# Kernel optimization log

Hardware: AMD Instinct MI355X
Metric: run time of the kernel (lower is better)

Reference implementation:

```python
import jax, jax.numpy as jnp
import numpy as np
from jax import lax

D_MODEL = 2048
D_INNER = 4096  # expand * d_model
D_CONV = 4
B, T = 4, 2048


def _rmsnorm(h):
    # F.normalize(x, dim=-1) * sqrt(D): x / max(||x||_2, 1e-12) * sqrt(D)
    n = jnp.sqrt(jnp.sum(h * h, axis=-1, keepdims=True))
    return h / jnp.maximum(n, 1e-12) * (h.shape[-1] ** 0.5)


def setup_inputs() -> dict:
    key = jax.random.key(0)
    ks = jax.random.split(key, 7)
    std = 0.02
    return {
        "x": jax.random.normal(ks[0], (B, T, D_MODEL), jnp.float32),
        "W_in": jax.random.normal(ks[1], (2 * D_INNER, D_MODEL), jnp.float32) * std,
        "conv_w": jax.random.normal(ks[2], (D_INNER, 1, D_CONV), jnp.float32) * std,
        "conv_b": jnp.zeros((D_INNER,), jnp.float32),
        "W_out": jax.random.normal(ks[3], (D_MODEL, D_INNER), jnp.float32) * std,
        "W_mlp1": jax.random.normal(ks[4], (4 * D_MODEL, D_MODEL), jnp.float32) * std,
        "W_mlp2": jax.random.normal(ks[5], (D_MODEL, 4 * D_MODEL), jnp.float32) * std,
    }


def _mamba_fallback(h, W_in, conv_w, conv_b, W_out):
    # in_proj: (B,T,D) -> (B,T,2*d_inner), split into x branch and gate z
    xz = jnp.einsum("btd,ed->bte", h, W_in)
    xp, z = jnp.split(xz, 2, axis=-1)
    # depthwise causal conv over time: torch pads (d_conv-1) both sides then slices [:T]
    # == left-pad-only causal cross-correlation
    xc = lax.conv_general_dilated(
        xp.transpose(0, 2, 1),  # (B, d_inner, T)
        conv_w,                  # (d_inner, 1, d_conv)
        window_strides=(1,),
        padding=[(D_CONV - 1, 0)],
        dimension_numbers=("NCH", "OIH", "NCH"),
        feature_group_count=D_INNER,
    ) + conv_b[None, :, None]
    xc = xc.transpose(0, 2, 1)  # (B, T, d_inner)
    y = jax.nn.silu(xc) * jax.nn.silu(z)
    return jnp.einsum("bte,de->btd", y, W_out)


def reference(x, W_in, conv_w, conv_b, W_out, W_mlp1, W_mlp2):
    # full-dimension path (active_dim=None)
    h = _rmsnorm(x)
    x = x + _mamba_fallback(h, W_in, conv_w, conv_b, W_out)
    h = _rmsnorm(x)
    m = jnp.einsum("bte,de->btd", jax.nn.relu(jnp.einsum("btd,ed->bte", h, W_mlp1)), W_mlp2)
    return x + m
```

## Files before the change

kernel.cpp:

```cpp
#include <hip/hip_runtime.h>
#include <hip/hip_bf16.h>

typedef __bf16 bf16;
typedef __bf16 bf16x8 __attribute__((ext_vector_type(8)));
typedef __bf16 bf16x4 __attribute__((ext_vector_type(4)));
typedef float f32x4 __attribute__((ext_vector_type(4)));

#define D_MODEL 2048
#define D_INNER 4096
#define ROWS    8192

__device__ __forceinline__ void gload_lds16(const void* g, void* l) {
    __builtin_amdgcn_global_load_lds(
        (const __attribute__((address_space(1))) void*)g,
        (__attribute__((address_space(3))) void*)l, 16, 0, 0);
}

__device__ __forceinline__ void f2b_body(const float* __restrict__ in,
                                         bf16* __restrict__ out, int i, int n8) {
    if (i >= n8) return;
    long base = (long)i * 8;
    float4 a = *(const float4*)(in + base);
    float4 b = *(const float4*)(in + base + 4);
    bf16x8 o;
    o[0] = (bf16)a.x; o[1] = (bf16)a.y; o[2] = (bf16)a.z; o[3] = (bf16)a.w;
    o[4] = (bf16)b.x; o[5] = (bf16)b.y; o[6] = (bf16)b.z; o[7] = (bf16)b.w;
    *(bf16x8*)(out + base) = o;
}

__device__ __forceinline__ void rmsnorm_body(const float* __restrict__ x,
                                             bf16* __restrict__ h, int row) {
    const float* xr = x + (long)row * D_MODEL;
    float4 v0 = ((const float4*)xr)[threadIdx.x * 2];
    float4 v1 = ((const float4*)xr)[threadIdx.x * 2 + 1];
    float ss = v0.x*v0.x + v0.y*v0.y + v0.z*v0.z + v0.w*v0.w
             + v1.x*v1.x + v1.y*v1.y + v1.z*v1.z + v1.w*v1.w;
    #pragma unroll
    for (int o = 32; o; o >>= 1) ss += __shfl_xor(ss, o, 64);
    __shared__ float red[4];
    if ((threadIdx.x & 63) == 0) red[threadIdx.x >> 6] = ss;
    __syncthreads();
    float tot = red[0] + red[1] + red[2] + red[3];
    float scale = 45.254834f / fmaxf(sqrtf(tot), 1e-12f);
    bf16x8 o;
    o[0] = (bf16)(v0.x*scale); o[1] = (bf16)(v0.y*scale);
    o[2] = (bf16)(v0.z*scale); o[3] = (bf16)(v0.w*scale);
    o[4] = (bf16)(v1.x*scale); o[5] = (bf16)(v1.y*scale);
    o[6] = (bf16)(v1.z*scale); o[7] = (bf16)(v1.w*scale);
    *(bf16x8*)(h + (long)row * D_MODEL + threadIdx.x * 8) = o;
}

__device__ __forceinline__ void rmsnorm_body_b16(const bf16* __restrict__ x,
                                                 bf16* __restrict__ h, int row) {
    const bf16* xr = x + (long)row * D_MODEL;
    bf16x8 v = *(const bf16x8*)(xr + threadIdx.x * 8);
    float f[8];
    float ss = 0.f;
    #pragma unroll
    for (int e = 0; e < 8; ++e) { f[e] = (float)v[e]; ss += f[e] * f[e]; }
    #pragma unroll
    for (int o = 32; o; o >>= 1) ss += __shfl_xor(ss, o, 64);
    __shared__ float red[4];
    if ((threadIdx.x & 63) == 0) red[threadIdx.x >> 6] = ss;
    __syncthreads();
    float tot = red[0] + red[1] + red[2] + red[3];
    float scale = 45.254834f / fmaxf(sqrtf(tot), 1e-12f);
    bf16x8 o;
    #pragma unroll
    for (int e = 0; e < 8; ++e) o[e] = (bf16)(f[e] * scale);
    *(bf16x8*)(h + (long)row * D_MODEL + threadIdx.x * 8) = o;
}

__device__ __forceinline__ void conv_body(bf16* __restrict__ xz,
                                          const float* __restrict__ cw,
                                          const float* __restrict__ cb, int idx) {
    const int c8  = idx & 511;
    const int row = idx >> 9;
    const int t   = row & 2047;
    const int c0  = c8 * 8;
    float acc[8];
    float wv[8][4];
    #pragma unroll
    for (int e = 0; e < 8; ++e) {
        float4 f = ((const float4*)cw)[c0 + e];
        wv[e][0] = f.x; wv[e][1] = f.y; wv[e][2] = f.z; wv[e][3] = f.w;
        acc[e] = cb[c0 + e];
    }
    #pragma unroll
    for (int j = 0; j < 4; ++j) {
        if (t + j - 3 >= 0) {
            bf16x8 xv = *(const bf16x8*)(xz + (long)(row + j - 3) * (2*D_INNER) + c0);
            #pragma unroll
            for (int e = 0; e < 8; ++e) acc[e] += (float)xv[e] * wv[e][j];
        }
    }
    bf16* zp = xz + (long)row * (2*D_INNER) + D_INNER + c0;
    bf16x8 zv = *(const bf16x8*)zp;
    bf16x8 yv;
    #pragma unroll
    for (int e = 0; e < 8; ++e) {
        float xc = acc[e];
        float s1 = xc / (1.f + __expf(-xc));
        float z  = (float)zv[e];
        float s2 = z / (1.f + __expf(-z));
        yv[e] = (bf16)(s1 * s2);
    }
    *(bf16x8*)zp = yv;
}

__global__ __launch_bounds__(256) void prep_kernel(const float* __restrict__ x,
                                                   bf16* __restrict__ h,
                                                   const float* __restrict__ w,
                                                   bf16* __restrict__ wOut, int n8) {
    if ((int)blockIdx.x < ROWS) rmsnorm_body(x, h, blockIdx.x);
    else f2b_body(w, wOut, (blockIdx.x - ROWS) * 256 + threadIdx.x, n8);
}

__global__ __launch_bounds__(256) void prep2_kernel(const bf16* __restrict__ x2b,
                                                    bf16* __restrict__ h,
                                                    const float* __restrict__ w1,
                                                    bf16* __restrict__ w1o,
                                                    const float* __restrict__ w2,
                                                    bf16* __restrict__ w2o, int n8) {
    if ((int)blockIdx.x < ROWS) rmsnorm_body_b16(x2b, h, blockIdx.x);
    else if ((int)blockIdx.x < 2 * ROWS)
        f2b_body(w1, w1o, (blockIdx.x - ROWS) * 256 + threadIdx.x, n8);
    else
        f2b_body(w2, w2o, (blockIdx.x - 2 * ROWS) * 256 + threadIdx.x, n8);
}

__global__ __launch_bounds__(256) void convf2b_kernel(bf16* __restrict__ xz,
                                                      const float* __restrict__ cw,
                                                      const float* __restrict__ cb,
                                                      const float* __restrict__ w,
                                                      bf16* __restrict__ wOut, int n8) {
    if ((int)blockIdx.x < 16384) conv_body(xz, cw, cb, blockIdx.x * 256 + threadIdx.x);
    else f2b_body(w, wOut, (blockIdx.x - 16384) * 256 + threadIdx.x, n8);
}

template<int EPI>
__global__ __launch_bounds__(512, 2) void gemm_bt(
        const bf16* __restrict__ A, long lda,
        const bf16* __restrict__ B,
        void* __restrict__ C, const void* __restrict__ res,
        int N, int K, int gx) {
    __shared__ __align__(16) char LB[131072];
    const int tid = threadIdx.x;
    const int w   = tid >> 6;
    const int l   = tid & 63;
    const int lr  = l & 15;

    int bx, by;
    if (gx == 32) {
        const int xcd = blockIdx.x & 7, i = blockIdx.x >> 3;
        by = (xcd >> 1) * 8 + (i >> 4);
        bx = (xcd & 1) * 16 + (i & 15);
    } else {
        const int qq = gridDim.x >> 3;
        const int sw = (blockIdx.x & 7) * qq + (blockIdx.x >> 3);
        bx = sw % gx; by = sw / gx;
    }
    const long rowBase = (long)by * 256;
    const long colBase = (long)bx * 256;

    const int srow = w * 8 + (l >> 3);
    const int schk = (l & 7) ^ ((l >> 3) & 7);
    const bf16* aSrc = A + (rowBase + srow) * lda + schk * 8;
    const bf16* bSrc = B + (colBase + srow) * (long)K + schk * 8;
    const long lda64 = 64 * lda;
    const long ldb64 = 64 * (long)K;
    const int  w1024 = w * 1024;

    auto stgA0 = [&](int DBB, int kt) {
        const bf16* s = aSrc + (long)kt * 64;
        gload_lds16(s,            LB + DBB +     0 + w1024);
        gload_lds16(s +   lda64,  LB + DBB +  8192 + w1024);
    };
    auto stgA1 = [&](int DBB, int kt) {
        const bf16* s = aSrc + (long)kt * 64;
        gload_lds16(s + 2*lda64,  LB + DBB + 16384 + w1024);
        gload_lds16(s + 3*lda64,  LB + DBB + 24576 + w1024);
    };
    auto stgB0 = [&](int DBB, int kt) {
        const bf16* s = bSrc + (long)kt * 64;
        gload_lds16(s,            LB + DBB + 32768 + w1024);
        gload_lds16(s +   ldb64,  LB + DBB + 40960 + w1024);
    };
    auto stgB1 = [&](int DBB, int kt) {
        const bf16* s = bSrc + (long)kt * 64;
        gload_lds16(s + 2*ldb64,  LB + DBB + 49152 + w1024);
        gload_lds16(s + 3*ldb64,  LB + DBB + 57344 + w1024);
    };

    const int cx0 = (((l >> 4)    ) ^ (l & 7)) << 4;
    const int cx1 = (((l >> 4) + 4) ^ (l & 7)) << 4;
    const int hm = w >> 2;
    const int q  = w & 3;
    int aRow[8], bRow[4];
    #pragma unroll
    for (int m = 0; m < 8; ++m) aRow[m] = hm * 16384 + (m * 16 + lr) * 128;
    #pragma unroll
    for (int n = 0; n < 4; ++n)
        bRow[n] = 32768 + (q >> 1) * 16384 + ((q & 1) * 64 + n * 16 + lr) * 128;

    const int nt  = K >> 6;
    const int nit = nt >> 1;
    f32x4 acc[8][4] = {};
    bf16x8 AX[4][2], BL[2][2], BH[2][2];

    stgB0(0, 0); stgB1(0, 0); stgA0(0, 0); stgA1(0, 0);
    stgB0(65536, 1); stgB1(65536, 1); stgA0(65536, 1); stgA1(65536, 1);
    asm volatile("s_waitcnt vmcnt(8)" ::: "memory");
    __builtin_amdgcn_s_barrier();
    __builtin_amdgcn_sched_barrier(0);
    #pragma unroll
    for (int m = 0; m < 4; ++m) {
        AX[m][0] = *(const bf16x8*)(LB + aRow[m] + cx0);
        AX[m][1] = *(const bf16x8*)(LB + aRow[m] + cx1);
    }
    #pragma unroll
    for (int n = 0; n < 2; ++n) {
        BL[n][0] = *(const bf16x8*)(LB + bRow[n]     + cx0);
        BL[n][1] = *(const bf16x8*)(LB + bRow[n]     + cx1);
    }
    #pragma unroll
    for (int n = 0; n < 2; ++n) {
        BH[n][0] = *(const bf16x8*)(LB + bRow[n + 2] + cx0);
        BH[n][1] = *(const bf16x8*)(LB + bRow[n + 2] + cx1);
    }
    asm volatile("s_waitcnt lgkmcnt(4)" ::: "memory");
    __builtin_amdgcn_sched_barrier(0);
    __builtin_amdgcn_s_setprio(1);
    #pragma unroll
    for (int m = 0; m < 4; ++m)
        #pragma unroll
        for (int n = 0; n < 2; ++n) {
            acc[m][n] = __builtin_amdgcn_mfma_f32_16x16x32_bf16(AX[m][0], BL[n][0], acc[m][n], 0, 0, 0);
            acc[m][n] = __builtin_amdgcn_mfma_f32_16x16x32_bf16(AX[m][1], BL[n][1], acc[m][n], 0, 0, 0);
        }
    __builtin_amdgcn_s_setprio(0);
    __builtin_amdgcn_s_barrier();

    for (int it = 0; it < nit; ++it) {
        int kA = 2 * it + 2; if (kA >= nt) kA = 0;
        int kB = 2 * it + 3; if (kB >= nt) kB = 0;
        #pragma unroll
        for (int db = 0; db < 2; ++db) {
            const int DBB = db * 65536;
            const char* Lb = LB + DBB;
            const char* Ln = LB + (DBB ^ 65536);
            const int kst = db ? kB : kA;
            const bool full = (db == 0) || (it < nit - 1);

            stgB0(DBB, kst);
            __builtin_amdgcn_s_setprio(1);
            #pragma unroll
            for (int m = 0; m < 4; ++m) {
                #pragma unroll
                for (int n = 0; n < 2; ++n) {
                    acc[m][n + 2] = __builtin_amdgcn_mfma_f32_16x16x32_bf16(AX[m][0], BH[n][0], acc[m][n + 2], 0, 0, 0);
                    acc[m][n + 2] = __builtin_amdgcn_mfma_f32_16x16x32_bf16(AX[m][1], BH[n][1], acc[m][n + 2], 0, 0, 0);
                }
                AX[m][0] = *(const bf16x8*)(Lb + aRow[m + 4] + cx0);
                AX[m][1] = *(const bf16x8*)(Lb + aRow[m + 4] + cx1);
            }
            __builtin_amdgcn_s_setprio(0);
            stgB1(DBB, kst);
            asm volatile("s_waitcnt lgkmcnt(0)" ::: "memory");
            __builtin_amdgcn_sched_barrier(0);
            __builtin_amdgcn_s_setprio(1);
            #pragma unroll
            for (int m = 0; m < 4; ++m)
                #pragma unroll
                for (int n = 0; n < 2; ++n) {
                    acc[m + 4][n + 2] = __builtin_amdgcn_mfma_f32_16x16x32_bf16(AX[m][0], BH[n][0], acc[m + 4][n + 2], 0, 0, 0);
                    acc[m + 4][n + 2] = __builtin_amdgcn_mfma_f32_16x16x32_bf16(AX[m][1], BH[n][1], acc[m + 4][n + 2], 0, 0, 0);
                }
            __builtin_amdgcn_s_setprio(0);
            asm volatile("s_waitcnt vmcnt(4)" ::: "memory");
            __builtin_amdgcn_s_barrier();
            __builtin_amdgcn_sched_barrier(0);

            __builtin_amdgcn_s_setprio(1);
            #pragma unroll
            for (int m = 0; m < 4; ++m) {
                #pragma unroll
                for (int n = 0; n < 2; ++n) {
                    acc[m + 4][n] = __builtin_amdgcn_mfma_f32_16x16x32_bf16(AX[m][0], BL[n][0], acc[m + 4][n], 0, 0, 0);
                    acc[m + 4][n] = __builtin_amdgcn_mfma_f32_16x16x32_bf16(AX[m][1], BL[n][1], acc[m + 4][n], 0, 0, 0);
                }
                if (full) {
                    AX[m][0] = *(const bf16x8*)(Ln + aRow[m] + cx0);
                    AX[m][1] = *(const bf16x8*)(Ln + aRow[m] + cx1);
                    if (m < 2) {
                        BH[m][0] = *(const bf16x8*)(Ln + bRow[m + 2] + cx0);
                        BH[m][1] = *(const bf16x8*)(Ln + bRow[m + 2] + cx1);
                    }
                }
            }
            __builtin_amdgcn_s_setprio(0);
            __builtin_amdgcn_sched_barrier(0);
            stgA0(DBB, kst);
            if (full) {
                #pragma unroll
                for (int n = 0; n < 2; ++n) {
                    BL[n][0] = *(const bf16x8*)(Ln + bRow[n]     + cx0);
                    BL[n][1] = *(const bf16x8*)(Ln + bRow[n]     + cx1);
                }
            }
            stgA1(DBB, kst);
            if (full) {
                asm volatile("s_waitcnt lgkmcnt(0)" ::: "memory");
                __builtin_amdgcn_sched_barrier(0);
                __builtin_amdgcn_s_setprio(1);
                #pragma unroll
                for (int m = 0; m < 4; ++m)
                    #pragma unroll
                    for (int n = 0; n < 2; ++n) {
                        acc[m][n] = __builtin_amdgcn_mfma_f32_16x16x32_bf16(AX[m][0], BL[n][0], acc[m][n], 0, 0, 0);
                        acc[m][n] = __builtin_amdgcn_mfma_f32_16x16x32_bf16(AX[m][1], BL[n][1], acc[m][n], 0, 0, 0);
                    }
                __builtin_amdgcn_s_setprio(0);
            }
            __builtin_amdgcn_s_barrier();
        }
    }

    asm volatile("s_waitcnt vmcnt(0)" ::: "memory");
    __builtin_amdgcn_s_barrier();

    const int lg = l >> 4;
    const long wrow = rowBase + hm * 128;
    const long wcol = colBase + q * 64;
    char* ep = LB + w * 16384;

    if (EPI == 3) {
        const bf16* rb = (const bf16*)res;
        #pragma unroll
        for (int mh = 0; mh < 2; ++mh) {
            #pragma unroll
            for (int m = 0; m < 4; ++m) {
                #pragma unroll
                for (int n = 0; n < 4; ++n) {
                    f32x4 v = acc[mh * 4 + m][n];
                    #pragma unroll
                    for (int r = 0; r < 4; ++r) {
                        int rowr = m * 16 + lg * 4 + r;
                        int chnk = (n * 4 + (lr >> 2)) ^ (rowr & 7);
                        *(float*)(ep + rowr * 256 + chnk * 16 + (lr & 3) * 4) = v[r];
                    }
                }
            }
            asm volatile("s_waitcnt lgkmcnt(0)" ::: "memory");
            #pragma unroll
            for (int i = 0; i < 16; ++i) {
                int rr = i * 4 + (l >> 4);
                float4 lv = *(float4*)(ep + rr * 256 + (((l & 15) ^ (rr & 7)) * 16));
                long off = (wrow + mh * 64 + rr) * N + wcol + (l & 15) * 4;
                bf16x4 rv = *(const bf16x4*)(rb + off);
                lv.x += (float)rv[0]; lv.y += (float)rv[1];
                lv.z += (float)rv[2]; lv.w += (float)rv[3];
                *(float4*)((float*)C + off) = lv;
            }
            if (mh == 0) { asm volatile("s_waitcnt lgkmcnt(0) vmcnt(0)" ::: "memory"); }
        }
    } else {
        const float* rf = (const float*)res;
        #pragma unroll
        for (int m = 0; m < 8; ++m) {
            #pragma unroll
            for (int n = 0; n < 4; ++n) {
                f32x4 v = acc[m][n];
                #pragma unroll
                for (int r = 0; r < 4; ++r) {
                    int rowr = m * 16 + lg * 4 + r;
                    int chnk = (n * 2 + (lr >> 3)) ^ (rowr & 7);
                    float val = v[r];
                    if (EPI == 1) val = fmaxf(val, 0.f);
                    if (EPI == 2) val += rf[(wrow + rowr) * N + wcol + n * 16 + lr];
                    *(bf16*)(ep + rowr * 128 + chnk * 16 + (lr & 7) * 2) = (bf16)val;
                }
            }
        }
        asm volatile("s_waitcnt lgkmcnt(0)" ::: "memory");
        #pragma unroll
        for (int i = 0; i < 16; ++i) {
            int rr = i * 8 + (l >> 3);
            uint4 lv = *(uint4*)(ep + rr * 128 + (((l & 7) ^ (rr & 7)) * 16));
            *(uint4*)((bf16*)C + (wrow + rr) * N + wcol + (l & 7) * 8) = lv;
        }
    }
}

extern "C" void kernel_launch(void* const* d_in, const int* in_sizes, int n_in,
                              void* d_out, int out_size, void* d_ws, size_t ws_size,
                              hipStream_t stream) {
    const float* x      = (const float*)d_in[0];
    const float* W_in   = (const float*)d_in[1];
    const float* cw     = (const float*)d_in[2];
    const float* cb     = (const float*)d_in[3];
    const float* W_out  = (const float*)d_in[4];
    const float* W_mlp1 = (const float*)d_in[5];
    const float* W_mlp2 = (const float*)d_in[6];
    float* out = (float*)d_out;

    char* ws  = (char*)d_ws;
    bf16* wW  = (bf16*)(ws);
    bf16* h   = (bf16*)(ws + 33554432);
    bf16* xz  = (bf16*)(ws + 67108864);
    bf16* x2b = (bf16*)(ws + 201326592);
    bf16* wW2 = (bf16*)(ws + 234881024);
    bf16* y   = xz + D_INNER;
    bf16* m1  = xz;

    dim3 blk(256);
    dim3 gblk(512);

    prep_kernel<<<dim3(ROWS + 8192), blk, 0, stream>>>(x, h, W_in, wW, 16777216/8);
    gemm_bt<0><<<dim3(1024), gblk, 0, stream>>>(h, D_MODEL, wW, xz, nullptr, 2*D_INNER, D_MODEL, 32);
    convf2b_kernel<<<dim3(16384 + 4096), blk, 0, stream>>>(xz, cw, cb, W_out, wW, 8388608/8);
    gemm_bt<2><<<dim3(256), gblk, 0, stream>>>(y, 2*D_INNER, wW, x2b, x, D_MODEL, D_INNER, 8);

    prep2_kernel<<<dim3(3 * ROWS), blk, 0, stream>>>(x2b, h, W_mlp1, wW, W_mlp2, wW2, 16777216/8);
    gemm_bt<1><<<dim3(1024), gblk, 0, stream>>>(h, D_MODEL, wW, m1, nullptr, 4*D_MODEL, D_MODEL, 32);
    gemm_bt<3><<<dim3(256), gblk, 0, stream>>>(m1, 4*D_MODEL, wW2, out, x2b, D_MODEL, 4*D_MODEL, 8);
}
```

Measured before the change: 934.2 us.

## Shrink GEMM tiles to 128x128 with 256-thread blocks and simpler pipeline

Reworks the bf16 MFMA GEMM from 256x256 tiles with 8 waves and 128KB LDS to 128x128 tiles with 4 waves and 64KB LDS. The grid grows fourfold and the XCD-aware tile mapping is generalised. The interleaved half-tile load and MFMA schedule is replaced with a simpler per-stage ordering. The goal is better occupancy and wave-count balance on the N=2048 GEMMs, which previously launched only 256 blocks. The cost is lower arithmetic intensity per tile and more global/L2 traffic for the A and B operands.

```diff
diff --git a/kernel.cpp b/kernel.cpp
--- a/kernel.cpp
+++ b/kernel.cpp
@@ -139,77 +139,66 @@
 }
 
 template<int EPI>
-__global__ __launch_bounds__(512, 2) void gemm_bt(
+__global__ __launch_bounds__(256, 2) void gemm_bt(
         const bf16* __restrict__ A, long lda,
         const bf16* __restrict__ B,
         void* __restrict__ C, const void* __restrict__ res,
         int N, int K, int gx) {
-    __shared__ __align__(16) char LB[131072];
+    __shared__ __align__(16) char LB[65536];
     const int tid = threadIdx.x;
     const int w   = tid >> 6;
     const int l   = tid & 63;
     const int lr  = l & 15;
 
-    int bx, by;
-    if (gx == 32) {
-        const int xcd = blockIdx.x & 7, i = blockIdx.x >> 3;
-        by = (xcd >> 1) * 8 + (i >> 4);
-        bx = (xcd & 1) * 16 + (i & 15);
-    } else {
-        const int qq = gridDim.x >> 3;
-        const int sw = (blockIdx.x & 7) * qq + (blockIdx.x >> 3);
-        bx = sw % gx; by = sw / gx;
-    }
-    const long rowBase = (long)by * 256;
-    const long colBase = (long)bx * 256;
+    const int nwg = gridDim.x;
+    const int xcd = blockIdx.x & 7, i = blockIdx.x >> 3;
+    const int hw  = gx >> 1;
+    const int rh  = (nwg >> 3) / hw;
+    const int by  = (xcd >> 1) * rh + i / hw;
+    const int bx  = (xcd & 1) * hw + i % hw;
+    const long rowBase = (long)by * 128;
+    const long colBase = (long)bx * 128;
 
     const int srow = w * 8 + (l >> 3);
     const int schk = (l & 7) ^ ((l >> 3) & 7);
     const bf16* aSrc = A + (rowBase + srow) * lda + schk * 8;
     const bf16* bSrc = B + (colBase + srow) * (long)K + schk * 8;
-    const long lda64 = 64 * lda;
-    const long ldb64 = 64 * (long)K;
+    const long lda32 = 32 * lda;
+    const long ldb32 = 32 * (long)K;
     const int  w1024 = w * 1024;
 
-    auto stgA0 = [&](int DBB, int kt) {
+    auto stgA = [&](int DBB, int kt) {
         const bf16* s = aSrc + (long)kt * 64;
         gload_lds16(s,            LB + DBB +     0 + w1024);
-        gload_lds16(s +   lda64,  LB + DBB +  8192 + w1024);
+        gload_lds16(s +   lda32,  LB + DBB +  4096 + w1024);
+        gload_lds16(s + 2*lda32,  LB + DBB +  8192 + w1024);
+        gload_lds16(s + 3*lda32,  LB + DBB + 12288 + w1024);
     };
-    auto stgA1 = [&](int DBB, int kt) {
-        const bf16* s = aSrc + (long)kt * 64;
-        gload_lds16(s + 2*lda64,  LB + DBB + 16384 + w1024);
-        gload_lds16(s + 3*lda64,  LB + DBB + 24576 + w1024);
-    };
-    auto stgB0 = [&](int DBB, int kt) {
+    auto stgB = [&](int DBB, int kt) {
         const bf16* s = bSrc + (long)kt * 64;
-        gload_lds16(s,            LB + DBB + 32768 + w1024);
-        gload_lds16(s +   ldb64,  LB + DBB + 40960 + w1024);
-    };
-    auto stgB1 = [&](int DBB, int kt) {
-        const bf16* s = bSrc + (long)kt * 64;
-        gload_lds16(s + 2*ldb64,  LB + DBB + 49152 + w1024);
-        gload_lds16(s + 3*ldb64,  LB + DBB + 57344 + w1024);
+        gload_lds16(s,            LB + DBB + 16384 + w1024);
+        gload_lds16(s +   ldb32,  LB + DBB + 20480 + w1024);
+        gload_lds16(s + 2*ldb32,  LB + DBB + 24576 + w1024);
+        gload_lds16(s + 3*ldb32,  LB + DBB + 28672 + w1024);
     };
 
     const int cx0 = (((l >> 4)    ) ^ (l & 7)) << 4;
     const int cx1 = (((l >> 4) + 4) ^ (l & 7)) << 4;
-    const int hm = w >> 2;
-    const int q  = w & 3;
-    int aRow[8], bRow[4];
-    #pragma unroll
-    for (int m = 0; m < 8; ++m) aRow[m] = hm * 16384 + (m * 16 + lr) * 128;
-    #pragma unroll
-    for (int n = 0; n < 4; ++n)
-        bRow[n] = 32768 + (q >> 1) * 16384 + ((q & 1) * 64 + n * 16 + lr) * 128;
+    const int hm = w >> 1;
+    const int hn = w & 1;
+    int aRow[4], bRow[4];
+    #pragma unroll
+    for (int m = 0; m < 4; ++m) aRow[m] = (hm * 64 + m * 16 + lr) * 128;
+    #pragma unroll
+    for (int n = 0; n < 4; ++n) bRow[n] = 16384 + (hn * 64 + n * 16 + lr) * 128;
 
     const int nt  = K >> 6;
     const int nit = nt >> 1;
-    f32x4 acc[8][4] = {};
+    f32x4 acc[4][4] = {};
     bf16x8 AX[4][2], BL[2][2], BH[2][2];
 
-    stgB0(0, 0); stgB1(0, 0); stgA0(0, 0); stgA1(0, 0);
-    stgB0(65536, 1); stgB1(65536, 1); stgA0(65536, 1); stgA1(65536, 1);
+    stgB(0, 0);      stgA(0, 0);
+    stgB(32768, 1);  stgA(32768, 1);
     asm volatile("s_waitcnt vmcnt(8)" ::: "memory");
     __builtin_amdgcn_s_barrier();
     __builtin_amdgcn_sched_barrier(0);
@@ -239,78 +228,54 @@
             acc[m][n] = __builtin_amdgcn_mfma_f32_16x16x32_bf16(AX[m][1], BL[n][1], acc[m][n], 0, 0, 0);
         }
     __builtin_amdgcn_s_setprio(0);
+    asm volatile("s_waitcnt lgkmcnt(0)" ::: "memory");
     __builtin_amdgcn_s_barrier();
+    __builtin_amdgcn_sched_barrier(0);
 
     for (int it = 0; it < nit; ++it) {
         int kA = 2 * it + 2; if (kA >= nt) kA = 0;
         int kB = 2 * it + 3; if (kB >= nt) kB = 0;
         #pragma unroll
         for (int db = 0; db < 2; ++db) {
-            const int DBB = db * 65536;
-            const char* Lb = LB + DBB;
-            const char* Ln = LB + (DBB ^ 65536);
+            const int DBB = db * 32768;
+            const char* Ln = LB + (DBB ^ 32768);
             const int kst = db ? kB : kA;
             const bool full = (db == 0) || (it < nit - 1);
 
-            stgB0(DBB, kst);
+            stgB(DBB, kst);
             __builtin_amdgcn_s_setprio(1);
             #pragma unroll
-            for (int m = 0; m < 4; ++m) {
+            for (int m = 0; m < 4; ++m)
                 #pragma unroll
                 for (int n = 0; n < 2; ++n) {
                     acc[m][n + 2] = __builtin_amdgcn_mfma_f32_16x16x32_bf16(AX[m][0], BH[n][0], acc[m][n + 2], 0, 0, 0);
                     acc[m][n + 2] = __builtin_amdgcn_mfma_f32_16x16x32_bf16(AX[m][1], BH[n][1], acc[m][n + 2], 0, 0, 0);
-                }
-                AX[m][0] = *(const bf16x8*)(Lb + aRow[m + 4] + cx0);
-                AX[m][1] = *(const bf16x8*)(Lb + aRow[m + 4] + cx1);
-            }
-            __builtin_amdgcn_s_setprio(0);
-            stgB1(DBB, kst);
-            asm volatile("s_waitcnt lgkmcnt(0)" ::: "memory");
-            __builtin_amdgcn_sched_barrier(0);
-            __builtin_amdgcn_s_setprio(1);
-            #pragma unroll
-            for (int m = 0; m < 4; ++m)
-                #pragma unroll
-                for (int n = 0; n < 2; ++n) {
-                    acc[m + 4][n + 2] = __builtin_amdgcn_mfma_f32_16x16x32_bf16(AX[m][0], BH[n][0], acc[m + 4][n + 2], 0, 0, 0);
-                    acc[m + 4][n + 2] = __builtin_amdgcn_mfma_f32_16x16x32_bf16(AX[m][1], BH[n][1], acc[m + 4][n + 2], 0, 0, 0);
                 }
             __builtin_amdgcn_s_setprio(0);
             asm volatile("s_waitcnt vmcnt(4)" ::: "memory");
             __builtin_amdgcn_s_barrier();
             __builtin_amdgcn_sched_barrier(0);
 
-            __builtin_amdgcn_s_setprio(1);
-            #pragma unroll
-            for (int m = 0; m < 4; ++m) {
-                #pragma unroll
-                for (int n = 0; n < 2; ++n) {
-                    acc[m + 4][n] = __builtin_amdgcn_mfma_f32_16x16x32_bf16(AX[m][0], BL[n][0], acc[m + 4][n], 0, 0, 0);
-                    acc[m + 4][n] = __builtin_amdgcn_mfma_f32_16x16x32_bf16(AX[m][1], BL[n][1], acc[m + 4][n], 0, 0, 0);
-                }
-                if (full) {
+            if (full) {
+                #pragma unroll
+                for (int m = 0; m < 4; ++m) {
                     AX[m][0] = *(const bf16x8*)(Ln + aRow[m] + cx0);
                     AX[m][1] = *(const bf16x8*)(Ln + aRow[m] + cx1);
-                    if (m < 2) {
-                        BH[m][0] = *(const bf16x8*)(Ln + bRow[m + 2] + cx0);
-                        BH[m][1] = *(const bf16x8*)(Ln + bRow[m + 2] + cx1);
-                    }
-                }
-            }
-            __builtin_amdgcn_s_setprio(0);
-            __builtin_amdgcn_sched_barrier(0);
-            stgA0(DBB, kst);
-            if (full) {
+                }
                 #pragma unroll
                 for (int n = 0; n < 2; ++n) {
                     BL[n][0] = *(const bf16x8*)(Ln + bRow[n]     + cx0);
                     BL[n][1] = *(const bf16x8*)(Ln + bRow[n]     + cx1);
                 }
             }
-            stgA1(DBB, kst);
+            stgA(DBB, kst);
             if (full) {
-                asm volatile("s_waitcnt lgkmcnt(0)" ::: "memory");
+                #pragma unroll
+                for (int n = 0; n < 2; ++n) {
+                    BH[n][0] = *(const bf16x8*)(Ln + bRow[n + 2] + cx0);
+                    BH[n][1] = *(const bf16x8*)(Ln + bRow[n + 2] + cx1);
+                }
+                asm volatile("s_waitcnt lgkmcnt(4)" ::: "memory");
                 __builtin_amdgcn_sched_barrier(0);
                 __builtin_amdgcn_s_setprio(1);
                 #pragma unroll
@@ -321,8 +286,10 @@
                         acc[m][n] = __builtin_amdgcn_mfma_f32_16x16x32_bf16(AX[m][1], BL[n][1], acc[m][n], 0, 0, 0);
                     }
                 __builtin_amdgcn_s_setprio(0);
+                asm volatile("s_waitcnt lgkmcnt(0)" ::: "memory");
             }
             __builtin_amdgcn_s_barrier();
+            __builtin_amdgcn_sched_barrier(0);
         }
     }
 
@@ -330,44 +297,40 @@
     __builtin_amdgcn_s_barrier();
 
     const int lg = l >> 4;
-    const long wrow = rowBase + hm * 128;
-    const long wcol = colBase + q * 64;
+    const long wrow = rowBase + hm * 64;
+    const long wcol = colBase + hn * 64;
     char* ep = LB + w * 16384;
 
     if (EPI == 3) {
         const bf16* rb = (const bf16*)res;
         #pragma unroll
-        for (int mh = 0; mh < 2; ++mh) {
+        for (int m = 0; m < 4; ++m) {
             #pragma unroll
-            for (int m = 0; m < 4; ++m) {
-                #pragma unroll
-                for (int n = 0; n < 4; ++n) {
-                    f32x4 v = acc[mh * 4 + m][n];
-                    #pragma unroll
-                    for (int r = 0; r < 4; ++r) {
-                        int rowr = m * 16 + lg * 4 + r;
-                        int chnk = (n * 4 + (lr >> 2)) ^ (rowr & 7);
-                        *(float*)(ep + rowr * 256 + chnk * 16 + (lr & 3) * 4) = v[r];
-                    }
+            for (int n = 0; n < 4; ++n) {
+                f32x4 v = acc[m][n];
+                #pragma unroll
+                for (int r = 0; r < 4; ++r) {
+                    int rowr = m * 16 + lg * 4 + r;
+                    int chnk = (n * 4 + (lr >> 2)) ^ (rowr & 7);
+                    *(float*)(ep + rowr * 256 + chnk * 16 + (lr & 3) * 4) = v[r];
                 }
             }
-            asm volatile("s_waitcnt lgkmcnt(0)" ::: "memory");
-            #pragma unroll
-            for (int i = 0; i < 16; ++i) {
-                int rr = i * 4 + (l >> 4);
-                float4 lv = *(float4*)(ep + rr * 256 + (((l & 15) ^ (rr & 7)) * 16));
-                long off = (wrow + mh * 64 + rr) * N + wcol + (l & 15) * 4;
-                bf16x4 rv = *(const bf16x4*)(rb + off);
-                lv.x += (float)rv[0]; lv.y += (float)rv[1];
-                lv.z += (float)rv[2]; lv.w += (float)rv[3];
-                *(float4*)((float*)C + off) = lv;
-            }
-            if (mh == 0) { asm volatile("s_waitcnt lgkmcnt(0) vmcnt(0)" ::: "memory"); }
+        }
+        asm volatile("s_waitcnt lgkmcnt(0)" ::: "memory");
+        #pragma unroll
+        for (int i = 0; i < 16; ++i) {
+            int rr = i * 4 + (l >> 4);
+            float4 lv = *(float4*)(ep + rr * 256 + (((l & 15) ^ (rr & 7)) * 16));
+            long off = (wrow + rr) * N + wcol + (l & 15) * 4;
+            bf16x4 rv = *(const bf16x4*)(rb + off);
+            lv.x += (float)rv[0]; lv.y += (float)rv[1];
+            lv.z += (float)rv[2]; lv.w += (float)rv[3];
+            *(float4*)((float*)C + off) = lv;
         }
     } else {
         const float* rf = (const float*)res;
         #pragma unroll
-        for (int m = 0; m < 8; ++m) {
+        for (int m = 0; m < 4; ++m) {
             #pragma unroll
             for (int n = 0; n < 4; ++n) {
                 f32x4 v = acc[m][n];
@@ -384,7 +347,7 @@
         }
         asm volatile("s_waitcnt lgkmcnt(0)" ::: "memory");
         #pragma unroll
-        for (int i = 0; i < 16; ++i) {
+        for (int i = 0; i < 8; ++i) {
             int rr = i * 8 + (l >> 3);
             uint4 lv = *(uint4*)(ep + rr * 128 + (((l & 7) ^ (rr & 7)) * 16));
             *(uint4*)((bf16*)C + (wrow + rr) * N + wcol + (l & 7) * 8) = lv;
@@ -414,14 +377,13 @@
     bf16* m1  = xz;
 
     dim3 blk(256);
-    dim3 gblk(512);
 
     prep_kernel<<<dim3(ROWS + 8192), blk, 0, stream>>>(x, h, W_in, wW, 16777216/8);
-    gemm_bt<0><<<dim3(1024), gblk, 0, stream>>>(h, D_MODEL, wW, xz, nullptr, 2*D_INNER, D_MODEL, 32);
+    gemm_bt<0><<<dim3(4096), blk, 0, stream>>>(h, D_MODEL, wW, xz, nullptr, 2*D_INNER, D_MODEL, 64);
     convf2b_kernel<<<dim3(16384 + 4096), blk, 0, stream>>>(xz, cw, cb, W_out, wW, 8388608/8);
-    gemm_bt<2><<<dim3(256), gblk, 0, stream>>>(y, 2*D_INNER, wW, x2b, x, D_MODEL, D_INNER, 8);
+    gemm_bt<2><<<dim3(1024), blk, 0, stream>>>(y, 2*D_INNER, wW, x2b, x, D_MODEL, D_INNER, 16);
 
     prep2_kernel<<<dim3(3 * ROWS), blk, 0, stream>>>(x2b, h, W_mlp1, wW, W_mlp2, wW2, 16777216/8);
-    gemm_bt<1><<<dim3(1024), gblk, 0, stream>>>(h, D_MODEL, wW, m1, nullptr, 4*D_MODEL, D_MODEL, 32);
-    gemm_bt<3><<<dim3(256), gblk, 0, stream>>>(m1, 4*D_MODEL, wW2, out, x2b, D_MODEL, 4*D_MODEL, 8);
-}
+    gemm_bt<1><<<dim3(4096), blk, 0, stream>>>(h, D_MODEL, wW, m1, nullptr, 4*D_MODEL, D_MODEL, 64);
+    gemm_bt<3><<<dim3(1024), blk, 0, stream>>>(m1, 4*D_MODEL, wW2, out, x2b, D_MODEL, 4*D_MODEL, 16);
+}
```

Result: slower. 1.274 ms (+36.4%).
